# Performance work log

Hardware: AMD Instinct MI355X
Metric: run time of the kernel (lower is better)

## Reference

```python
import jax, jax.numpy as jnp
import numpy as np

B, S, D = 2, 2048, 2048
NH, NKV = 32, 8
HD = D // NH           # 64
GS = NH // NKV         # 4
ROPE_BASE = 10000.0


def _rope_tables(seq_len, head_dim, base):
    inv_freq = 1.0 / (base ** (jnp.arange(head_dim // 2, dtype=jnp.float32) / (head_dim // 2)))
    angles = jnp.arange(seq_len, dtype=jnp.float32)[:, None] * inv_freq[None, :]  # [S, HD/2]
    angles = jnp.concatenate([angles, angles], axis=-1)                            # [S, HD]
    return jnp.cos(angles), jnp.sin(angles)


def _apply_rope(x, cos, sin):
    # x: [B, H, S, HD]
    hd = x.shape[-1]
    x1, x2 = x[..., : hd // 2], x[..., hd // 2 :]
    rotated = jnp.concatenate([-x2, x1], axis=-1)
    return (x * cos[None, None] + rotated * sin[None, None]).astype(x.dtype)


def setup_inputs() -> dict:
    key = jax.random.key(0)
    ks = jax.random.split(key, 5)
    scale = 0.02
    return {
        "x": jax.random.normal(ks[0], (B, S, D), dtype=jnp.float32),
        "Wq": jax.random.normal(ks[1], (D, D), dtype=jnp.float32) * scale,
        "Wk": jax.random.normal(ks[2], (D, NKV * HD), dtype=jnp.float32) * scale,
        "Wv": jax.random.normal(ks[3], (D, NKV * HD), dtype=jnp.float32) * scale,
        "Wo": jax.random.normal(ks[4], (D, D), dtype=jnp.float32) * scale,
    }


def reference(x, Wq, Wk, Wv, Wo):
    b, n, _ = x.shape
    cos, sin = _rope_tables(n, HD, ROPE_BASE)

    q = (x @ Wq).reshape(b, n, NH, HD).transpose(0, 2, 1, 3)    # [B, NH, S, HD]
    k = (x @ Wk).reshape(b, n, NKV, HD).transpose(0, 2, 1, 3)   # [B, NKV, S, HD]
    v = (x @ Wv).reshape(b, n, NKV, HD).transpose(0, 2, 1, 3)

    q = _apply_rope(q, cos, sin)
    k = _apply_rope(k, cos, sin)

    # GQA head sharing: repeat_interleave KV groups to full head count
    k = jnp.repeat(k, GS, axis=1)   # [B, NH, S, HD]
    v = jnp.repeat(v, GS, axis=1)

    scores = jnp.einsum("bhqd,bhkd->bhqk", q, k)                # [B, NH, S, S]
    causal = jnp.triu(jnp.ones((n, n), dtype=bool), k=1)
    scores = jnp.where(causal[None, None], -jnp.inf, scores)
    weights = jax.nn.softmax(scores / jnp.sqrt(jnp.float32(HD)), axis=-1)

    ctx = jnp.einsum("bhqk,bhkd->bhqd", weights, v)             # [B, NH, S, HD]
    ctx = ctx.transpose(0, 2, 1, 3).reshape(b, n, D)
    return ctx @ Wo
```

## Files before the change

kernel.cpp:

```cpp
#include <hip/hip_runtime.h>

typedef __bf16 bf16;
typedef __attribute__((ext_vector_type(8))) __bf16 bf16x8;
typedef __attribute__((ext_vector_type(4))) float f32x4;
typedef __attribute__((ext_vector_type(4))) short s16x4;

#define S_LEN 2048
#define D_MODEL 2048
#define NHEADS 32
#define NKVH 8
#define HDIM 64
#define BATCH 2

__device__ __forceinline__ void async_cp16(const bf16* g, bf16* l) {
    __builtin_amdgcn_global_load_lds(
        (const __attribute__((address_space(1))) unsigned int*)g,
        (__attribute__((address_space(3))) unsigned int*)l, 16, 0, 0);
}

__global__ void cvt_f32_bf16(const float* __restrict__ in, bf16* __restrict__ out, int n4) {
    int i = blockIdx.x * blockDim.x + threadIdx.x;
    if (i < n4) {
        float4 f = ((const float4*)in)[i];
        union { bf16 h[4]; uint2 u; } t;
        t.h[0] = (bf16)f.x; t.h[1] = (bf16)f.y; t.h[2] = (bf16)f.z; t.h[3] = (bf16)f.w;
        ((uint2*)out)[i] = t.u;
    }
}

__global__ void transpose_w(const float* __restrict__ W, bf16* __restrict__ Wt, int K, int N) {
    __shared__ float tile[32][33];
    int kt = blockIdx.y * 32, nt = blockIdx.x * 32;
    int tx = threadIdx.x, ty = threadIdx.y;
    #pragma unroll
    for (int i = 0; i < 32; i += 8)
        tile[ty + i][tx] = W[(size_t)(kt + ty + i) * N + nt + tx];
    __syncthreads();
    #pragma unroll
    for (int i = 0; i < 32; i += 8)
        Wt[(size_t)(nt + ty + i) * K + kt + tx] = (bf16)tile[tx][ty + i];
}

__global__ void transpose_v(const bf16* __restrict__ QKV, bf16* __restrict__ Vt) {
    __shared__ bf16 tl[32][33];
    int z = blockIdx.z;
    int s0 = blockIdx.x * 32, d0 = blockIdx.y * 32;
    int bb = z >> 3, hh = z & 7;
    int tx = threadIdx.x, ty = threadIdx.y;
    #pragma unroll
    for (int i = 0; i < 32; i += 8)
        tl[ty + i][tx] = QKV[((size_t)(bb * S_LEN + s0 + ty + i)) * 3072 + 2560 + hh * 64 + d0 + tx];
    __syncthreads();
    #pragma unroll
    for (int i = 0; i < 32; i += 8)
        Vt[((size_t)z * 64 + d0 + ty + i) * S_LEN + s0 + tx] = tl[tx][ty + i];
}

template <bool OUT_BF16>
__global__ __launch_bounds__(256) void gemm_bt(const bf16* __restrict__ A,
                                               const bf16* __restrict__ Bt,
                                               void* __restrict__ Cv,
                                               int M, int N, int K) {
    __shared__ __align__(16) bf16 As[128 * 64];
    __shared__ __align__(16) bf16 Bs[128 * 64];

    const int tid  = threadIdx.x;
    const int wave = tid >> 6;
    const int lane = tid & 63;
    const int l16  = lane & 15;
    const int quad = lane >> 4;
    const int wrow = (wave >> 1) * 64;
    const int wcol = (wave & 1) * 64;
    const int m0 = blockIdx.y * 128;
    const int n0 = blockIdx.x * 128;

    const int krow = lane >> 3;
    const int kc   = (lane & 7) ^ krow;
    const bf16* gA = A  + (size_t)(m0 + wave * 32 + krow) * K + kc * 8;
    const bf16* gB = Bt + (size_t)(n0 + wave * 32 + krow) * K + kc * 8;
    bf16* lA = &As[wave * 2048];
    bf16* lB = &Bs[wave * 2048];
    const size_t rstep = (size_t)8 * K;

    const int sw = l16 & 7;

    f32x4 acc[4][4];
    #pragma unroll
    for (int mi = 0; mi < 4; ++mi)
        #pragma unroll
        for (int ni = 0; ni < 4; ++ni)
            acc[mi][ni] = (f32x4){0.f, 0.f, 0.f, 0.f};

    for (int k0 = 0; k0 < K; k0 += 64) {
        __syncthreads();
        async_cp16(gA,             lA);
        async_cp16(gA +     rstep, lA + 512);
        async_cp16(gA + 2 * rstep, lA + 1024);
        async_cp16(gA + 3 * rstep, lA + 1536);
        async_cp16(gB,             lB);
        async_cp16(gB +     rstep, lB + 512);
        async_cp16(gB + 2 * rstep, lB + 1024);
        async_cp16(gB + 3 * rstep, lB + 1536);
        gA += 64; gB += 64;
        __syncthreads();

        #pragma unroll
        for (int kk = 0; kk < 2; ++kk) {
            bf16x8 af[4], bfr[4];
            #pragma unroll
            for (int mi = 0; mi < 4; ++mi)
                af[mi] = *(const bf16x8*)&As[(wrow + mi * 16 + l16) * 64 + (((kk * 4 + quad) ^ sw) * 8)];
            #pragma unroll
            for (int ni = 0; ni < 4; ++ni)
                bfr[ni] = *(const bf16x8*)&Bs[(wcol + ni * 16 + l16) * 64 + (((kk * 4 + quad) ^ sw) * 8)];
            #pragma unroll
            for (int mi = 0; mi < 4; ++mi)
                #pragma unroll
                for (int ni = 0; ni < 4; ++ni)
                    acc[mi][ni] = __builtin_amdgcn_mfma_f32_16x16x32_bf16(af[mi], bfr[ni], acc[mi][ni], 0, 0, 0);
        }
    }

    #pragma unroll
    for (int mi = 0; mi < 4; ++mi) {
        #pragma unroll
        for (int ni = 0; ni < 4; ++ni) {
            #pragma unroll
            for (int r = 0; r < 4; ++r) {
                size_t row = (size_t)(m0 + wrow + mi * 16 + quad * 4 + r);
                size_t col = (size_t)(n0 + wcol + ni * 16 + l16);
                if (OUT_BF16) ((bf16*)Cv)[row * N + col] = (bf16)acc[mi][ni][r];
                else          ((float*)Cv)[row * N + col] = acc[mi][ni][r];
            }
        }
    }
}

__global__ void rope_relayout(const bf16* __restrict__ QKV,
                              bf16* __restrict__ Qr, bf16* __restrict__ Kr) {
    const int QN = BATCH * S_LEN * NHEADS * 32;
    const int KN = BATCH * S_LEN * NKVH * 32;
    const float LC = 0.28782313662425572f;
    int idx = blockIdx.x * 256 + threadIdx.x;
    if (idx < QN) {
        int j = idx & 31, hh = (idx >> 5) & 31, s = (idx >> 10) & 2047, bb = idx >> 21;
        size_t src = ((size_t)(bb * S_LEN + s)) * 3072 + hh * HDIM + j;
        float x1 = (float)QKV[src], x2 = (float)QKV[src + 32];
        float ang = (float)s * __expf(-(float)j * LC);
        float sn, cs; sincosf(ang, &sn, &cs);
        size_t dst = ((size_t)((bb * NHEADS + hh) * S_LEN + s)) * HDIM + j;
        Qr[dst]      = (bf16)((x1 * cs - x2 * sn) * 0.125f);
        Qr[dst + 32] = (bf16)((x2 * cs + x1 * sn) * 0.125f);
    } else if (idx < QN + KN) {
        int t = idx - QN;
        int j = t & 31, hh = (t >> 5) & 7, s = (t >> 8) & 2047, bb = t >> 19;
        size_t src = ((size_t)(bb * S_LEN + s)) * 3072 + 2048 + hh * HDIM + j;
        float x1 = (float)QKV[src], x2 = (float)QKV[src + 32];
        float ang = (float)s * __expf(-(float)j * LC);
        float sn, cs; sincosf(ang, &sn, &cs);
        size_t dst = ((size_t)((bb * NKVH + hh) * S_LEN + s)) * HDIM + j;
        Kr[dst]      = (bf16)(x1 * cs - x2 * sn);
        Kr[dst + 32] = (bf16)(x2 * cs + x1 * sn);
    }
}

__global__ __launch_bounds__(256, 3) void attn_kernel(const bf16* __restrict__ Q,
                                                      const bf16* __restrict__ K,
                                                      const bf16* __restrict__ Vt,
                                                      bf16* __restrict__ Ctx) {
    __shared__ __align__(16) bf16 KsL[128 * 64];
    __shared__ __align__(16) bf16 VtL[64 * 128];

    static const signed char QTAB[16] = {15,14,13,12, 10,11,8,9, 5,4,7,6, 0,1,2,3};
    const int bx = blockIdx.x;
    const int qt = QTAB[((bx >> 8) << 2) | ((bx >> 6) & 3)];
    const int bh = bx & 63;
    const int b  = bh >> 5;
    const int h  = bh & 31;
    const int kvh = h >> 2;
    const int tid = threadIdx.x;
    const int wave = tid >> 6;
    const int lane = tid & 63;
    const int l16  = lane & 15;
    const int quad = lane >> 4;

    const bf16* Qb = Q  + ((size_t)(b * NHEADS + h)) * S_LEN * HDIM;
    const bf16* Kb = K  + ((size_t)(b * NKVH + kvh)) * S_LEN * HDIM;
    const bf16* Vb = Vt + ((size_t)(b * NKVH + kvh)) * HDIM * S_LEN;

    const int q0 = qt * 128;

    bf16x8 aq[2][2];
    #pragma unroll
    for (int qf = 0; qf < 2; ++qf)
        #pragma unroll
        for (int ks = 0; ks < 2; ++ks)
            aq[qf][ks] = *(const bf16x8*)(Qb + (size_t)(q0 + wave * 32 + qf * 16 + l16) * HDIM + ks * 32 + quad * 8);

    f32x4 O[2][4];
    float M0 = -1e30f, M1 = -1e30f;
    float l0 = 0.f, l1 = 0.f;
    #pragma unroll
    for (int qf = 0; qf < 2; ++qf)
        #pragma unroll
        for (int df = 0; df < 4; ++df) O[qf][df] = (f32x4){0.f,0.f,0.f,0.f};

    const int krow = lane >> 3, kslot = lane & 7;
    const int kc   = kslot ^ (krow & 7);
    const int vslot = lane & 15, vsub = lane >> 4;

    #pragma unroll 1
    for (int kt = 0; kt <= qt; ++kt) {
        const int k0 = kt * 128;
        __syncthreads();
        #pragma unroll
        for (int j = 0; j < 4; ++j) {
            int rbase = (wave * 4 + j) * 8;
            async_cp16(Kb + (size_t)(k0 + rbase + krow) * HDIM + kc * 8, &KsL[rbase * 64]);
            int d0 = (wave * 4 + j) * 4;
            int vrow = d0 + vsub;
            int vc = vslot ^ (vrow & 15);
            async_cp16(Vb + (size_t)vrow * S_LEN + k0 + vc * 8, &VtL[d0 * 128]);
        }
        __syncthreads();

        f32x4 sc[2][8];
        #pragma unroll
        for (int kf = 0; kf < 8; ++kf) {
            sc[0][kf] = (f32x4){0.f,0.f,0.f,0.f};
            sc[1][kf] = (f32x4){0.f,0.f,0.f,0.f};
            #pragma unroll
            for (int ks = 0; ks < 2; ++ks) {
                bf16x8 bk = *(const bf16x8*)&KsL[(kf * 16 + l16) * 64 + (((ks * 4 + quad) ^ (l16 & 7)) * 8)];
                sc[0][kf] = __builtin_amdgcn_mfma_f32_16x16x32_bf16(bk, aq[0][ks], sc[0][kf], 0, 0, 0);
                sc[1][kf] = __builtin_amdgcn_mfma_f32_16x16x32_bf16(bk, aq[1][ks], sc[1][kf], 0, 0, 0);
            }
        }

        if (kt == qt) {
            #pragma unroll
            for (int kf = 0; kf < 8; ++kf)
                #pragma unroll
                for (int r = 0; r < 4; ++r) {
                    int key = kf * 16 + quad * 4 + r;
                    int qi0 = wave * 32 + l16;
                    if (key > qi0)      sc[0][kf][r] = -1e30f;
                    if (key > qi0 + 16) sc[1][kf][r] = -1e30f;
                }
        }

        float mx0 = sc[0][0][0], mx1 = sc[1][0][0];
        #pragma unroll
        for (int kf = 0; kf < 8; ++kf)
            #pragma unroll
            for (int r = 0; r < 4; ++r) {
                mx0 = fmaxf(mx0, sc[0][kf][r]);
                mx1 = fmaxf(mx1, sc[1][kf][r]);
            }
        mx0 = fmaxf(mx0, __shfl_xor(mx0, 16)); mx0 = fmaxf(mx0, __shfl_xor(mx0, 32));
        mx1 = fmaxf(mx1, __shfl_xor(mx1, 16)); mx1 = fmaxf(mx1, __shfl_xor(mx1, 32));

        float Mn0 = fmaxf(M0, mx0), Mn1 = fmaxf(M1, mx1);
        float a0 = __expf(M0 - Mn0), a1 = __expf(M1 - Mn1);
        M0 = Mn0; M1 = Mn1;
        l0 *= a0; l1 *= a1;

        #pragma unroll
        for (int r = 0; r < 4; ++r) {
            float aO0 = __shfl(a0, quad * 4 + r);
            float aO1 = __shfl(a1, quad * 4 + r);
            #pragma unroll
            for (int df = 0; df < 4; ++df) {
                O[0][df][r] *= aO0;
                O[1][df][r] *= aO1;
            }
        }

        #pragma unroll
        for (int kf = 0; kf < 8; ++kf)
            #pragma unroll
            for (int r = 0; r < 4; ++r) {
                float e0 = __expf(sc[0][kf][r] - M0); sc[0][kf][r] = e0; l0 += e0;
                float e1 = __expf(sc[1][kf][r] - M1); sc[1][kf][r] = e1; l1 += e1;
            }

        #pragma unroll
        for (int kf = 0; kf < 8; ++kf) {
            union { bf16 hh[4]; s16x4 s4; } p0, p1;
            #pragma unroll
            for (int r = 0; r < 4; ++r) {
                p0.hh[r] = (bf16)sc[0][kf][r];
                p1.hh[r] = (bf16)sc[1][kf][r];
            }
            #pragma unroll
            for (int df = 0; df < 4; ++df) {
                s16x4 bv = *(const s16x4*)&VtL[(df * 16 + l16) * 128 +
                                               (((kf * 2 + (quad >> 1)) ^ l16) * 8) + (quad & 1) * 4];
                O[0][df] = __builtin_amdgcn_mfma_f32_16x16x16bf16_1k(p0.s4, bv, O[0][df], 0, 0, 0);
                O[1][df] = __builtin_amdgcn_mfma_f32_16x16x16bf16_1k(p1.s4, bv, O[1][df], 0, 0, 0);
            }
        }
    }

    l0 += __shfl_xor(l0, 16); l0 += __shfl_xor(l0, 32);
    l1 += __shfl_xor(l1, 16); l1 += __shfl_xor(l1, 32);
    #pragma unroll
    for (int r = 0; r < 4; ++r) {
        float inv0 = 1.0f / __shfl(l0, quad * 4 + r);
        float inv1 = 1.0f / __shfl(l1, quad * 4 + r);
        size_t row0 = (size_t)b * S_LEN + q0 + wave * 32 + quad * 4 + r;
        bf16* dst0 = Ctx + row0 * D_MODEL + h * HDIM;
        bf16* dst1 = dst0 + (size_t)16 * D_MODEL;
        #pragma unroll
        for (int df = 0; df < 4; ++df) {
            dst0[df * 16 + l16] = (bf16)(O[0][df][r] * inv0);
            dst1[df * 16 + l16] = (bf16)(O[1][df][r] * inv1);
        }
    }
}

extern "C" void kernel_launch(void* const* d_in, const int* in_sizes, int n_in,
                              void* d_out, int out_size, void* d_ws, size_t ws_size,
                              hipStream_t stream) {
    const float* x  = (const float*)d_in[0];
    const float* Wq = (const float*)d_in[1];
    const float* Wk = (const float*)d_in[2];
    const float* Wv = (const float*)d_in[3];
    const float* Wo = (const float*)d_in[4];

    char* p = (char*)d_ws;
    bf16* X16 = (bf16*)p; p += (size_t)4096 * 2048 * 2;
    bf16* WqT = (bf16*)p; p += (size_t)2048 * 2048 * 2;
    bf16* WkT = (bf16*)p; p += (size_t)512 * 2048 * 2;
    bf16* WvT = (bf16*)p; p += (size_t)512 * 2048 * 2;
    bf16* WoT = (bf16*)p; p += (size_t)2048 * 2048 * 2;
    bf16* QKV = (bf16*)p; p += (size_t)4096 * 3072 * 2;
    bf16* Qr  = (bf16*)p; p += (size_t)4096 * 2048 * 2;
    bf16* Kr  = (bf16*)p; p += (size_t)4096 * 512 * 2;
    bf16* Vt  = (bf16*)p; p += (size_t)16 * 64 * 2048 * 2;
    bf16* Ctx = QKV;

    cvt_f32_bf16<<<8192, 256, 0, stream>>>(x, X16, 2097152);
    transpose_w<<<dim3(64, 64), dim3(32, 8), 0, stream>>>(Wq, WqT, 2048, 2048);
    transpose_w<<<dim3(16, 64), dim3(32, 8), 0, stream>>>(Wk, WkT, 2048, 512);
    transpose_w<<<dim3(16, 64), dim3(32, 8), 0, stream>>>(Wv, WvT, 2048, 512);
    transpose_w<<<dim3(64, 64), dim3(32, 8), 0, stream>>>(Wo, WoT, 2048, 2048);

    gemm_bt<true><<<dim3(24, 32), 256, 0, stream>>>(X16, WqT, (void*)QKV, 4096, 3072, 2048);

    rope_relayout<<<20480, 256, 0, stream>>>(QKV, Qr, Kr);
    transpose_v<<<dim3(64, 2, 16), dim3(32, 8), 0, stream>>>(QKV, Vt);
    attn_kernel<<<1024, 256, 0, stream>>>(Qr, Kr, Vt, Ctx);

    gemm_bt<false><<<dim3(16, 32), 256, 0, stream>>>(Ctx, WoT, d_out, 4096, 2048, 2048);
}
```

Baseline: 299.8 us.

## Replace 128x128 GEMM with double-buffered 256x256 ping-pong pipelined kernel

Replaces the single-buffered 128x128-tile GEMM with a 512-thread, 256x256-tile kernel. It uses double-buffered LDS, staged async global-to-LDS loads interleaved between MFMA quadrants, s_setprio, and explicit vmcnt waits. It also remaps block IDs in an XCD-aware way for locality. The aim is to hide global load latency and raise data reuse per tile. In exchange it uses 128KB of LDS per block, adds register pressure, and only 192 and 128 blocks are launched, which may underfill the CUs.

Measured after the change: 321.0 us. 7.1% more time.

```diff
diff --git a/kernel.cpp b/kernel.cpp
--- a/kernel.cpp
+++ b/kernel.cpp
@@ -56,84 +56,148 @@
         Vt[((size_t)z * 64 + d0 + ty + i) * S_LEN + s0 + tx] = tl[tx][ty + i];
 }
 
+#define BUF1 16384
+
+#define VMW(n) asm volatile("s_waitcnt vmcnt(" #n ")" ::: "memory")
+
+#define STAGE_A0(BUFOFF) do { \
+    async_cp16(pa00, As + (BUFOFF) + la00); \
+    async_cp16(pa01, As + (BUFOFF) + la01); \
+    pa00 += 64; pa01 += 64; } while (0)
+#define STAGE_A1(BUFOFF) do { \
+    async_cp16(pa10, As + (BUFOFF) + la10); \
+    async_cp16(pa11, As + (BUFOFF) + la11); \
+    pa10 += 64; pa11 += 64; } while (0)
+#define STAGE_B0(BUFOFF) do { \
+    async_cp16(pb00, Bs + (BUFOFF) + lb00); \
+    async_cp16(pb01, Bs + (BUFOFF) + lb01); \
+    pb00 += 64; pb01 += 64; } while (0)
+#define STAGE_B1(BUFOFF) do { \
+    async_cp16(pb10, Bs + (BUFOFF) + lb10); \
+    async_cp16(pb11, Bs + (BUFOFF) + lb11); \
+    pb10 += 64; pb11 += 64; } while (0)
+
+#define READ_A(QM, BUFOFF) do { \
+    _Pragma("unroll") \
+    for (int m_ = 0; m_ < 4; ++m_) { \
+        const int row_ = wr * 128 + (QM) * 64 + m_ * 16 + l16; \
+        af[m_][0] = *(const bf16x8*)&As[(BUFOFF) + row_ * 64 + ((quad ^ sw8) * 8)]; \
+        af[m_][1] = *(const bf16x8*)&As[(BUFOFF) + row_ * 64 + (((4 + quad) ^ sw8) * 8)]; \
+    } } while (0)
+
+#define READ_B(QN, BUFOFF) do { \
+    _Pragma("unroll") \
+    for (int n_ = 0; n_ < 2; ++n_) { \
+        const int row_ = wc * 64 + (QN) * 32 + n_ * 16 + l16; \
+        bfr[n_][0] = *(const bf16x8*)&Bs[(BUFOFF) + row_ * 64 + ((quad ^ sw8) * 8)]; \
+        bfr[n_][1] = *(const bf16x8*)&Bs[(BUFOFF) + row_ * 64 + (((4 + quad) ^ sw8) * 8)]; \
+    } } while (0)
+
+#define MFMA_Q(QM, QN) do { \
+    _Pragma("unroll") \
+    for (int kk_ = 0; kk_ < 2; ++kk_) \
+        _Pragma("unroll") \
+        for (int m_ = 0; m_ < 4; ++m_) \
+            _Pragma("unroll") \
+            for (int n_ = 0; n_ < 2; ++n_) \
+                acc[(QM) * 4 + m_][(QN) * 2 + n_] = __builtin_amdgcn_mfma_f32_16x16x32_bf16( \
+                    af[m_][kk_], bfr[n_][kk_], acc[(QM) * 4 + m_][(QN) * 2 + n_], 0, 0, 0); \
+    } while (0)
+
+#define SYNC_MFMA(QM, QN) do { \
+    __builtin_amdgcn_s_barrier(); \
+    asm volatile("s_waitcnt lgkmcnt(0)" ::: "memory"); \
+    __builtin_amdgcn_sched_barrier(0); \
+    __builtin_amdgcn_s_setprio(1); \
+    MFMA_Q(QM, QN); \
+    __builtin_amdgcn_s_setprio(0); } while (0)
+
+#define TILE4(CUR, S1, S2, S3, S4, WAIT) \
+    READ_A(0, CUR); READ_B(0, CUR); S1; SYNC_MFMA(0, 0); __builtin_amdgcn_s_barrier(); \
+    READ_B(1, CUR);                 S2; SYNC_MFMA(0, 1); __builtin_amdgcn_s_barrier(); \
+    READ_A(1, CUR); READ_B(0, CUR); S3; SYNC_MFMA(1, 0); __builtin_amdgcn_s_barrier(); \
+    READ_B(1, CUR);                 S4; SYNC_MFMA(1, 1); WAIT; __builtin_amdgcn_s_barrier();
+
 template <bool OUT_BF16>
-__global__ __launch_bounds__(256) void gemm_bt(const bf16* __restrict__ A,
-                                               const bf16* __restrict__ Bt,
-                                               void* __restrict__ Cv,
-                                               int M, int N, int K) {
-    __shared__ __align__(16) bf16 As[128 * 64];
-    __shared__ __align__(16) bf16 Bs[128 * 64];
+__global__ __launch_bounds__(512, 2) void gemm256(const bf16* __restrict__ A,
+                                                  const bf16* __restrict__ Bt,
+                                                  void* __restrict__ Cv,
+                                                  int N, int K) {
+    __shared__ __align__(16) bf16 As[2 * 256 * 64];
+    __shared__ __align__(16) bf16 Bs[2 * 256 * 64];
 
     const int tid  = threadIdx.x;
-    const int wave = tid >> 6;
+    const int w    = tid >> 6;
     const int lane = tid & 63;
     const int l16  = lane & 15;
     const int quad = lane >> 4;
-    const int wrow = (wave >> 1) * 64;
-    const int wcol = (wave & 1) * 64;
-    const int m0 = blockIdx.y * 128;
-    const int n0 = blockIdx.x * 128;
+    const int sw8  = l16 & 7;
+    const int wr   = w >> 2;
+    const int wc   = w & 3;
+
+    const int nbx  = N >> 8;
+    const int nwg  = gridDim.x;
+    const int orig = blockIdx.x;
+    const int wg   = (orig & 7) * (nwg >> 3) + (orig >> 3);
+    const int n0   = (wg % nbx) * 256;
+    const int m0   = (wg / nbx) * 256;
 
     const int krow = lane >> 3;
     const int kc   = (lane & 7) ^ krow;
-    const bf16* gA = A  + (size_t)(m0 + wave * 32 + krow) * K + kc * 8;
-    const bf16* gB = Bt + (size_t)(n0 + wave * 32 + krow) * K + kc * 8;
-    bf16* lA = &As[wave * 2048];
-    bf16* lB = &Bs[wave * 2048];
-    const size_t rstep = (size_t)8 * K;
-
-    const int sw = l16 & 7;
-
-    f32x4 acc[4][4];
-    #pragma unroll
-    for (int mi = 0; mi < 4; ++mi)
+
+    const bf16* pa00 = A + (size_t)(m0 +   0 + w * 8 + krow) * K + kc * 8;
+    const bf16* pa01 = A + (size_t)(m0 + 128 + w * 8 + krow) * K + kc * 8;
+    const bf16* pa10 = A + (size_t)(m0 +  64 + w * 8 + krow) * K + kc * 8;
+    const bf16* pa11 = A + (size_t)(m0 + 192 + w * 8 + krow) * K + kc * 8;
+    const int brow0 = (w >> 2) * 64 + (w & 3) * 8 + krow;
+    const bf16* pb00 = Bt + (size_t)(n0 +       brow0) * K + kc * 8;
+    const bf16* pb01 = Bt + (size_t)(n0 + 128 + brow0) * K + kc * 8;
+    const bf16* pb10 = Bt + (size_t)(n0 +  32 + brow0) * K + kc * 8;
+    const bf16* pb11 = Bt + (size_t)(n0 + 160 + brow0) * K + kc * 8;
+
+    const int la00 = w * 512;
+    const int la01 = 8192 + w * 512;
+    const int la10 = 4096 + w * 512;
+    const int la11 = 12288 + w * 512;
+    const int lbb  = ((w >> 2) * 64 + (w & 3) * 8) * 64;
+    const int lb00 = lbb;
+    const int lb01 = 8192 + lbb;
+    const int lb10 = 2048 + lbb;
+    const int lb11 = 10240 + lbb;
+
+    f32x4 acc[8][4];
+    #pragma unroll
+    for (int i = 0; i < 8; ++i)
+        #pragma unroll
+        for (int j = 0; j < 4; ++j) acc[i][j] = (f32x4){0.f, 0.f, 0.f, 0.f};
+
+    bf16x8 af[4][2];
+    bf16x8 bfr[2][2];
+
+    STAGE_A0(0); STAGE_B0(0); STAGE_A1(0); STAGE_B1(0);
+    STAGE_A0(BUF1); STAGE_B0(BUF1);
+    VMW(4);
+    __builtin_amdgcn_s_barrier();
+
+    const int NITER = K >> 7;
+    for (int it = 0; it < NITER - 1; ++it) {
+        TILE4(0,    STAGE_A1(BUF1), STAGE_B1(BUF1), STAGE_A0(0),    STAGE_B0(0),    VMW(4))
+        TILE4(BUF1, STAGE_A1(0),    STAGE_B1(0),    STAGE_A0(BUF1), STAGE_B0(BUF1), VMW(4))
+    }
+    TILE4(0,    STAGE_A1(BUF1), STAGE_B1(BUF1), , , VMW(0))
+    TILE4(BUF1, , , , , )
+
+    #pragma unroll
+    for (int mi = 0; mi < 8; ++mi)
         #pragma unroll
         for (int ni = 0; ni < 4; ++ni)
-            acc[mi][ni] = (f32x4){0.f, 0.f, 0.f, 0.f};
-
-    for (int k0 = 0; k0 < K; k0 += 64) {
-        __syncthreads();
-        async_cp16(gA,             lA);
-        async_cp16(gA +     rstep, lA + 512);
-        async_cp16(gA + 2 * rstep, lA + 1024);
-        async_cp16(gA + 3 * rstep, lA + 1536);
-        async_cp16(gB,             lB);
-        async_cp16(gB +     rstep, lB + 512);
-        async_cp16(gB + 2 * rstep, lB + 1024);
-        async_cp16(gB + 3 * rstep, lB + 1536);
-        gA += 64; gB += 64;
-        __syncthreads();
-
-        #pragma unroll
-        for (int kk = 0; kk < 2; ++kk) {
-            bf16x8 af[4], bfr[4];
-            #pragma unroll
-            for (int mi = 0; mi < 4; ++mi)
-                af[mi] = *(const bf16x8*)&As[(wrow + mi * 16 + l16) * 64 + (((kk * 4 + quad) ^ sw) * 8)];
-            #pragma unroll
-            for (int ni = 0; ni < 4; ++ni)
-                bfr[ni] = *(const bf16x8*)&Bs[(wcol + ni * 16 + l16) * 64 + (((kk * 4 + quad) ^ sw) * 8)];
-            #pragma unroll
-            for (int mi = 0; mi < 4; ++mi)
-                #pragma unroll
-                for (int ni = 0; ni < 4; ++ni)
-                    acc[mi][ni] = __builtin_amdgcn_mfma_f32_16x16x32_bf16(af[mi], bfr[ni], acc[mi][ni], 0, 0, 0);
-        }
-    }
-
-    #pragma unroll
-    for (int mi = 0; mi < 4; ++mi) {
-        #pragma unroll
-        for (int ni = 0; ni < 4; ++ni) {
             #pragma unroll
             for (int r = 0; r < 4; ++r) {
-                size_t row = (size_t)(m0 + wrow + mi * 16 + quad * 4 + r);
-                size_t col = (size_t)(n0 + wcol + ni * 16 + l16);
+                size_t row = (size_t)(m0 + wr * 128 + mi * 16 + quad * 4 + r);
+                size_t col = (size_t)(n0 + wc * 64 + ni * 16 + l16);
                 if (OUT_BF16) ((bf16*)Cv)[row * N + col] = (bf16)acc[mi][ni][r];
                 else          ((float*)Cv)[row * N + col] = acc[mi][ni][r];
             }
-        }
-    }
 }
 
 __global__ void rope_relayout(const bf16* __restrict__ QKV,
@@ -346,11 +410,11 @@
     transpose_w<<<dim3(16, 64), dim3(32, 8), 0, stream>>>(Wv, WvT, 2048, 512);
     transpose_w<<<dim3(64, 64), dim3(32, 8), 0, stream>>>(Wo, WoT, 2048, 2048);
 
-    gemm_bt<true><<<dim3(24, 32), 256, 0, stream>>>(X16, WqT, (void*)QKV, 4096, 3072, 2048);
+    gemm256<true><<<dim3(192), 512, 0, stream>>>(X16, WqT, (void*)QKV, 3072, 2048);
 
     rope_relayout<<<20480, 256, 0, stream>>>(QKV, Qr, Kr);
     transpose_v<<<dim3(64, 2, 16), dim3(32, 8), 0, stream>>>(QKV, Vt);
     attn_kernel<<<1024, 256, 0, stream>>>(Qr, Kr, Vt, Ctx);
 
-    gemm_bt<false><<<dim3(16, 32), 256, 0, stream>>>(Ctx, WoT, d_out, 4096, 2048, 2048);
-}
+    gemm256<false><<<dim3(128), 512, 0, stream>>>(Ctx, WoT, d_out, 2048, 2048);
+}
```
